# Kernel optimization log

Hardware: AMD Instinct MI355X
Metric: run time of the kernel (lower is better)

Reference implementation:

```python
import jax, jax.numpy as jnp
import numpy as np

N_NODES = 50000
N_EDGES = 800000
F_IN = 32
H = 128
LN_EPS = 1e-5


def _gcn_layer(h, src, tgt, w_self, b_self, w_neigh, b_neigh):
    # h: [N, D]; src/tgt: [E]
    n = h.shape[0]
    self_feat = h @ w_self + b_self                      # [N, Dout]
    src_feat = h[src]                                    # [E, D] gather
    agg = jax.ops.segment_sum(src_feat, tgt, num_segments=n)          # [N, D]
    cnt = jax.ops.segment_sum(jnp.ones((src.shape[0],), h.dtype), tgt,
                              num_segments=n)[:, None]   # [N, 1]
    agg = agg / jnp.maximum(cnt, 1.0)
    return self_feat + agg @ w_neigh + b_neigh


def _layer_norm(x, gamma, beta):
    mu = jnp.mean(x, axis=-1, keepdims=True)
    var = jnp.mean(jnp.square(x - mu), axis=-1, keepdims=True)
    return (x - mu) * jax.lax.rsqrt(var + LN_EPS) * gamma + beta


def setup_inputs() -> dict:
    key = jax.random.key(0)
    ks = jax.random.split(key, 16)
    s_in = 1.0 / np.sqrt(F_IN)
    s_h = 1.0 / np.sqrt(H)
    inp = {
        "x": jax.random.normal(ks[0], (N_NODES, F_IN), jnp.float32),
        "edge_index": jax.random.randint(ks[1], (2, N_EDGES), 0, N_NODES, jnp.int64)
        if jax.config.jax_enable_x64 else
        jax.random.randint(ks[1], (2, N_EDGES), 0, N_NODES, jnp.int32),
        "w_in": jax.random.uniform(ks[2], (F_IN, H), jnp.float32, -s_in, s_in),
        "b_in": jax.random.uniform(ks[3], (H,), jnp.float32, -s_in, s_in),
        "ws0": jax.random.uniform(ks[4], (H, H), jnp.float32, -s_h, s_h),
        "bs0": jax.random.uniform(ks[5], (H,), jnp.float32, -s_h, s_h),
        "wn0": jax.random.uniform(ks[6], (H, H), jnp.float32, -s_h, s_h),
        "bn0": jax.random.uniform(ks[7], (H,), jnp.float32, -s_h, s_h),
        "g0": jnp.ones((H,), jnp.float32),
        "be0": jnp.zeros((H,), jnp.float32),
        "ws1": jax.random.uniform(ks[8], (H, H), jnp.float32, -s_h, s_h),
        "bs1": jax.random.uniform(ks[9], (H,), jnp.float32, -s_h, s_h),
        "wn1": jax.random.uniform(ks[10], (H, H), jnp.float32, -s_h, s_h),
        "bn1": jax.random.uniform(ks[11], (H,), jnp.float32, -s_h, s_h),
        "g1": jnp.ones((H,), jnp.float32),
        "be1": jnp.zeros((H,), jnp.float32),
    }
    return inp


def reference(x, edge_index, w_in, b_in, ws0, bs0, wn0, bn0, g0, be0,
              ws1, bs1, wn1, bn1, g1, be1):
    src, tgt = edge_index[0], edge_index[1]
    h = jax.nn.relu(x @ w_in + b_in)                     # input_proj + relu
    # layer 0 (intermediate): gcn -> LN -> relu -> dropout(eval=id) -> residual
    residual = h
    h = _gcn_layer(h, src, tgt, ws0, bs0, wn0, bn0)
    h = _layer_norm(h, g0, be0)
    h = jax.nn.relu(h) + residual
    # layer 1 (final): gcn -> LN
    h = _gcn_layer(h, src, tgt, ws1, bs1, wn1, bn1)
    h = _layer_norm(h, g1, be1)
    return h
```

## Files before the change

kernel.cpp:

```cpp
#include <hip/hip_runtime.h>

#define H 128
#define CAP 64
typedef unsigned short ushort_t;
typedef __bf16 bf16x8 __attribute__((ext_vector_type(8)));
typedef unsigned short u16x8 __attribute__((ext_vector_type(8)));
typedef float f32x4 __attribute__((ext_vector_type(4)));
typedef float f32x2 __attribute__((ext_vector_type(2)));

__device__ __forceinline__ float bf2f(ushort_t b) {
    return __uint_as_float(((unsigned int)b) << 16);
}
__device__ __forceinline__ ushort_t f2bf(float f) {
    unsigned int u = __float_as_uint(f);
    unsigned int r = (u + 0x7fffu + ((u >> 16) & 1u)) >> 16;
    return (ushort_t)r;
}
__device__ __forceinline__ unsigned char f2fp8(float f) {
    int r = __builtin_amdgcn_cvt_pk_fp8_f32(f, f, 0, false);
    return (unsigned char)(r & 0xff);
}
__device__ __forceinline__ void acc8(float* s, uint2 v) {
    f32x2 a0 = __builtin_amdgcn_cvt_pk_f32_fp8(v.x, false);
    f32x2 a1 = __builtin_amdgcn_cvt_pk_f32_fp8(v.x, true);
    f32x2 a2 = __builtin_amdgcn_cvt_pk_f32_fp8(v.y, false);
    f32x2 a3 = __builtin_amdgcn_cvt_pk_f32_fp8(v.y, true);
    s[0] += a0.x; s[1] += a0.y; s[2] += a1.x; s[3] += a1.y;
    s[4] += a2.x; s[5] += a2.y; s[6] += a3.x; s[7] += a3.y;
}

__device__ __forceinline__
void pack_one(int idx, const float* __restrict__ W0, const float* __restrict__ W1,
              const float* __restrict__ b0, const float* __restrict__ b1,
              ushort_t* __restrict__ Wpack, float* __restrict__ bsum,
              int Ksplit, int K)
{
    int total = K * 16;
    if (idx < total) {
        int l = idx & 63, tt = (idx >> 6) & 7, s = idx >> 9;
        int c = tt * 16 + (l & 15);
        int kb = s * 32 + ((l >> 4) & 3) * 8;
#pragma unroll
        for (int j = 0; j < 8; ++j) {
            int k = kb + j;
            float v = (k < Ksplit) ? W0[(size_t)k * H + c]
                                   : W1[(size_t)(k - Ksplit) * H + c];
            Wpack[(size_t)idx * 8 + j] = f2bf(v);
        }
    }
    if (idx < H) bsum[idx] = b0[idx] + (b1 ? b1[idx] : 0.f);
}

__global__ __launch_bounds__(256)
void k_prep(const float* __restrict__ w_in, const float* __restrict__ b_in,
            const float* __restrict__ ws0, const float* __restrict__ bs0,
            const float* __restrict__ wn0, const float* __restrict__ bn0,
            const float* __restrict__ ws1, const float* __restrict__ bs1,
            const float* __restrict__ wn1, const float* __restrict__ bn1,
            ushort_t* __restrict__ Wpin, float* __restrict__ bin,
            ushort_t* __restrict__ Wp0, float* __restrict__ bsm0,
            ushort_t* __restrict__ Wp1, float* __restrict__ bsm1,
            int* __restrict__ fl, int N)
{
    int b = blockIdx.x, t = threadIdx.x;
    if (b < 2) {
        pack_one(b * 256 + t, w_in, w_in, b_in, nullptr, Wpin, bin, 32, 32);
    } else if (b < 18) {
        pack_one((b - 2) * 256 + t, ws0, wn0, bs0, bn0, Wp0, bsm0, 128, 256);
    } else if (b < 34) {
        pack_one((b - 18) * 256 + t, ws1, wn1, bs1, bn1, Wp1, bsm1, 128, 256);
    } else {
        int i = (b - 34) * 256 + t;
        if (i < N) fl[i] = 0;
    }
}

#define FILL_CHUNK 4096

__device__ __forceinline__
void fill_body(int blk, const int* __restrict__ srcs, const int* __restrict__ tgts,
               int* __restrict__ fl, ushort_t* __restrict__ col, int E)
{
    int range = blk & 7;
    int chunk = blk >> 3;
    int lim = chunk * FILL_CHUNK + FILL_CHUNK;
    if (lim > E) lim = E;
    for (int i = chunk * FILL_CHUNK + threadIdx.x; i < lim; i += 256) {
        int tt = tgts[i];
        if ((tt >> 13) == range) {
            int p = atomicAdd(&fl[tt], 1);
            if (p < CAP) col[tt * CAP + p] = (ushort_t)srcs[i];
        }
    }
}

template<int K, int DO_LN, int RESREL, int RELU, int OUTBF, int HQ, int AF32>
__device__ __forceinline__
void gemm_body(int bidm,
               const ushort_t* __restrict__ A, const float* __restrict__ Af, int lda,
               const ushort_t* __restrict__ Wpack,
               const float* __restrict__ bias,
               const float* __restrict__ g, const float* __restrict__ be,
               const ushort_t* __restrict__ resid, int ldr,
               float* __restrict__ Cf, ushort_t* __restrict__ Cb,
               unsigned char* __restrict__ hq, int ldc, int M)
{
    constexpr int NS = K / 32;
    __shared__ ushort_t Bs[NS * 8 * 64 * 8];
    const int t = threadIdx.x;
    {
        const uint4* wsrc = (const uint4*)Wpack;
        uint4* wdst = (uint4*)Bs;
        constexpr int CH = K * 16;
#pragma unroll
        for (int i = t; i < CH; i += 256) wdst[i] = wsrc[i];
    }
    __syncthreads();

    const int wave = t >> 6, lane = t & 63;
    const int quad = lane >> 4, l16 = lane & 15;
    const int m0 = bidm * 128 + wave * 32;

    f32x4 acc[2][8];
#pragma unroll
    for (int mt = 0; mt < 2; ++mt)
#pragma unroll
        for (int nt = 0; nt < 8; ++nt) acc[mt][nt] = (f32x4){0.f, 0.f, 0.f, 0.f};

    bf16x8 afrag[NS][2];
#pragma unroll
    for (int s = 0; s < NS; ++s)
#pragma unroll
        for (int mt = 0; mt < 2; ++mt) {
            int row = m0 + mt * 16 + l16;
            if (row >= M) row = M - 1;
            if (AF32) {
                const float* p = Af + (size_t)row * lda + s * 32 + quad * 8;
                float4 v0 = *(const float4*)p;
                float4 v1 = *(const float4*)(p + 4);
                union { u16x8 u; bf16x8 b; } cv;
                cv.u[0] = f2bf(v0.x); cv.u[1] = f2bf(v0.y);
                cv.u[2] = f2bf(v0.z); cv.u[3] = f2bf(v0.w);
                cv.u[4] = f2bf(v1.x); cv.u[5] = f2bf(v1.y);
                cv.u[6] = f2bf(v1.z); cv.u[7] = f2bf(v1.w);
                afrag[s][mt] = cv.b;
            } else {
                afrag[s][mt] = *(const bf16x8*)(A + (size_t)row * lda + s * 32 + quad * 8);
            }
        }

    const bf16x8* bfr = (const bf16x8*)Bs;
#pragma unroll
    for (int s = 0; s < NS; ++s)
#pragma unroll
        for (int nt = 0; nt < 8; ++nt) {
            bf16x8 b = bfr[(s * 8 + nt) * 64 + lane];
#pragma unroll
            for (int mt = 0; mt < 2; ++mt)
                acc[mt][nt] = __builtin_amdgcn_mfma_f32_16x16x32_bf16(
                    afrag[s][mt], b, acc[mt][nt], 0, 0, 0);
        }

    float bv[8], gv[8], bev[8];
#pragma unroll
    for (int nt = 0; nt < 8; ++nt) {
        int c = nt * 16 + l16;
        bv[nt] = bias[c];
        if (DO_LN) { gv[nt] = g[c]; bev[nt] = be[c]; }
    }

#pragma unroll
    for (int mt = 0; mt < 2; ++mt)
#pragma unroll
        for (int r = 0; r < 4; ++r) {
            int row = m0 + mt * 16 + quad * 4 + r;
            float v[8];
#pragma unroll
            for (int nt = 0; nt < 8; ++nt) v[nt] = acc[mt][nt][r] + bv[nt];
            if (DO_LN) {
                float s1 = 0.f, s2 = 0.f;
#pragma unroll
                for (int nt = 0; nt < 8; ++nt) { s1 += v[nt]; s2 += v[nt] * v[nt]; }
#pragma unroll
                for (int mk = 1; mk < 16; mk <<= 1) {
                    s1 += __shfl_xor(s1, mk);
                    s2 += __shfl_xor(s2, mk);
                }
                float mu = s1 * (1.f / H);
                float var = s2 * (1.f / H) - mu * mu;
                float rs = rsqrtf(var + 1e-5f);
#pragma unroll
                for (int nt = 0; nt < 8; ++nt)
                    v[nt] = (v[nt] - mu) * rs * gv[nt] + bev[nt];
            }
            if (row < M) {
#pragma unroll
                for (int nt = 0; nt < 8; ++nt) {
                    int c = nt * 16 + l16;
                    float y = v[nt];
                    if (RELU) y = fmaxf(y, 0.f);
                    if (RESREL)
                        y = fmaxf(y, 0.f) + bf2f(resid[(size_t)row * ldr + c]);
                    if (OUTBF) Cb[(size_t)row * ldc + c] = f2bf(y);
                    else       Cf[(size_t)row * ldc + c] = y;
                    if (HQ) hq[(size_t)row * H + c] = f2fp8(y);
                }
            }
        }
}

__global__ __launch_bounds__(256)
void k_gin(const float* __restrict__ x, const ushort_t* __restrict__ Wpin,
           const float* __restrict__ bin,
           ushort_t* __restrict__ Cb, unsigned char* __restrict__ hq,
           const int* __restrict__ srcs, const int* __restrict__ tgts,
           int* __restrict__ fl, ushort_t* __restrict__ col, int E,
           int fillBlocks, int M)
{
    if ((int)blockIdx.x < fillBlocks) {
        fill_body(blockIdx.x, srcs, tgts, fl, col, E);
        return;
    }
    gemm_body<32, 0, 0, 1, 1, 1, 1>(blockIdx.x - fillBlocks,
        nullptr, x, 32, Wpin, bin, nullptr, nullptr, nullptr, 0,
        nullptr, Cb, hq, 256, M);
}

__global__ __launch_bounds__(256)
void k_gl0(const ushort_t* __restrict__ A, const ushort_t* __restrict__ Wp,
           const float* __restrict__ bias,
           const float* __restrict__ g, const float* __restrict__ be,
           ushort_t* __restrict__ Cb, unsigned char* __restrict__ hq, int M)
{
    gemm_body<256, 1, 1, 0, 1, 1, 0>(blockIdx.x,
        A, nullptr, 256, Wp, bias, g, be, A, 256,
        nullptr, Cb, hq, 256, M);
}

__global__ __launch_bounds__(256)
void k_gl1(const ushort_t* __restrict__ A, const ushort_t* __restrict__ Wp,
           const float* __restrict__ bias,
           const float* __restrict__ g, const float* __restrict__ be,
           float* __restrict__ Cf, int M)
{
    gemm_body<256, 1, 0, 0, 0, 0, 0>(blockIdx.x,
        A, nullptr, 256, Wp, bias, g, be, nullptr, 0,
        Cf, nullptr, nullptr, H, M);
}

__device__ __forceinline__
void agg_body(int blk, const unsigned char* __restrict__ hq,
              const int* __restrict__ fl,
              const ushort_t* __restrict__ col, ushort_t* __restrict__ out, int n)
{
    int wave = threadIdx.x >> 6;
    int lane = threadIdx.x & 63;
    int grp = lane >> 4, li = lane & 15;
    int n0 = blk * 8 + wave * 2;
    if (n0 >= n) return;

    int cnt[2], m[2];
#pragma unroll
    for (int u = 0; u < 2; ++u) {
        int nd = n0 + u;
        cnt[u] = (nd < n) ? fl[nd] : 0;
        m[u] = cnt[u] < CAP ? cnt[u] : CAP;
    }
    float s[2][8];
#pragma unroll
    for (int u = 0; u < 2; ++u)
#pragma unroll
        for (int j = 0; j < 8; ++j) s[u][j] = 0.f;

    int mx = m[0] > m[1] ? m[0] : m[1];
    for (int e = 0; e < mx; e += 16) {
        uint2 v[2][4];
#pragma unroll
        for (int u = 0; u < 2; ++u)
#pragma unroll
            for (int q = 0; q < 4; ++q) {
                int idx = e + q * 4 + grp;
                bool val = idx < m[u];
                int r = val ? (int)col[(n0 + u) * CAP + idx] : 0;
                uint2 tv = {0u, 0u};
                if (val) tv = *(const uint2*)(hq + (size_t)r * 128 + li * 8);
                v[u][q] = tv;
            }
#pragma unroll
        for (int u = 0; u < 2; ++u)
#pragma unroll
            for (int q = 0; q < 4; ++q) acc8(s[u], v[u][q]);
    }
#pragma unroll
    for (int u = 0; u < 2; ++u)
#pragma unroll
        for (int j = 0; j < 8; ++j) {
            s[u][j] += __shfl_xor(s[u][j], 16);
            s[u][j] += __shfl_xor(s[u][j], 32);
        }
    if (grp < 2 && (n0 + grp) < n) {
        int u = grp;
        float inv = 1.f / fmaxf((float)cnt[u], 1.f);
        uint4 o;
        o.x = ((unsigned)f2bf(s[u][1] * inv) << 16) | f2bf(s[u][0] * inv);
        o.y = ((unsigned)f2bf(s[u][3] * inv) << 16) | f2bf(s[u][2] * inv);
        o.z = ((unsigned)f2bf(s[u][5] * inv) << 16) | f2bf(s[u][4] * inv);
        o.w = ((unsigned)f2bf(s[u][7] * inv) << 16) | f2bf(s[u][6] * inv);
        *(uint4*)(out + (size_t)(n0 + u) * 256 + li * 8) = o;
    }
}

__global__ __launch_bounds__(256)
void k_agg0(const unsigned char* __restrict__ hq, const int* __restrict__ fl,
            const ushort_t* __restrict__ col, ushort_t* __restrict__ out, int n)
{ agg_body(blockIdx.x, hq, fl, col, out, n); }

__global__ __launch_bounds__(256)
void k_agg1(const unsigned char* __restrict__ hq, const int* __restrict__ fl,
            const ushort_t* __restrict__ col, ushort_t* __restrict__ out, int n)
{ agg_body(blockIdx.x, hq, fl, col, out, n); }

extern "C" void kernel_launch(void* const* d_in, const int* in_sizes, int n_in,
                              void* d_out, int out_size, void* d_ws, size_t ws_size,
                              hipStream_t stream)
{
    const float* x    = (const float*)d_in[0];
    const int*   ei   = (const int*)d_in[1];
    const float* w_in = (const float*)d_in[2];
    const float* b_in = (const float*)d_in[3];
    const float* ws0  = (const float*)d_in[4];
    const float* bs0  = (const float*)d_in[5];
    const float* wn0  = (const float*)d_in[6];
    const float* bn0  = (const float*)d_in[7];
    const float* g0   = (const float*)d_in[8];
    const float* be0  = (const float*)d_in[9];
    const float* ws1  = (const float*)d_in[10];
    const float* bs1  = (const float*)d_in[11];
    const float* wn1  = (const float*)d_in[12];
    const float* bn1  = (const float*)d_in[13];
    const float* g1   = (const float*)d_in[14];
    const float* be1  = (const float*)d_in[15];

    const int N = in_sizes[0] / 32;
    const int E = in_sizes[1] / 2;
    const int* srcs = ei;
    const int* tgts = ei + E;

    char* w = (char*)d_ws;
    ushort_t* Acat0 = (ushort_t*)w;  w += (size_t)N * 256 * 2;
    ushort_t* Acat1 = (ushort_t*)w;  w += (size_t)N * 256 * 2;
    unsigned char* hq0 = (unsigned char*)w;  w += (size_t)N * H;
    unsigned char* hq1 = (unsigned char*)w;  w += (size_t)N * H;
    ushort_t* Wpin  = (ushort_t*)w;  w += 32 * H * 2;
    ushort_t* Wp0   = (ushort_t*)w;  w += 256 * H * 2;
    ushort_t* Wp1   = (ushort_t*)w;  w += 256 * H * 2;
    float* bin  = (float*)w;         w += H * 4;
    float* bsm0 = (float*)w;         w += H * 4;
    float* bsm1 = (float*)w;         w += H * 4;
    int* fl     = (int*)w;           w += (size_t)N * 4;
    ushort_t* col = (ushort_t*)w;    w += (size_t)N * CAP * 2;

    int gN = (N + 255) / 256;
    int gM = (N + 127) / 128;
    int gA = (N + 7) / 8;
    int gF = 8 * ((E + FILL_CHUNK - 1) / FILL_CHUNK);

    k_prep<<<34 + gN, 256, 0, stream>>>(
        w_in, b_in, ws0, bs0, wn0, bn0, ws1, bs1, wn1, bn1,
        Wpin, bin, Wp0, bsm0, Wp1, bsm1, fl, N);

    k_gin<<<gF + gM, 256, 0, stream>>>(
        x, Wpin, bin, Acat0, hq0, srcs, tgts, fl, col, E, gF, N);

    k_agg0<<<gA, 256, 0, stream>>>(hq0, fl, col, Acat0 + 128, N);
    k_gl0<<<gM, 256, 0, stream>>>(Acat0, Wp0, bsm0, g0, be0, Acat1, hq1, N);

    k_agg1<<<gA, 256, 0, stream>>>(hq1, fl, col, Acat1 + 128, N);
    k_gl1<<<gM, 256, 0, stream>>>(Acat1, Wp1, bsm1, g1, be1, (float*)d_out, N);
}
```

Before: 233.9 us.

## Fuse neighbor aggregation into the layer GEMM via shared-memory tile

Drops the separate aggregation kernels. Each layer kernel now gathers fp8 neighbor features for 64 rows, writes the bf16 means into a swizzled shared-memory tile, and feeds them straight to the MFMA GEMM together with the self features. This removes two launches and the global round trip of the aggregated half of the concatenated activation, and the activation buffers shrink to width H. In exchange each block does only a 64-row tile with 64KB of staged weights plus 16KB for the tile, which lowers occupancy, and the per-thread serial gather loop has less memory-level parallelism than the old wave-parallel edge split.

```diff
diff --git a/kernel.cpp b/kernel.cpp
--- a/kernel.cpp
+++ b/kernel.cpp
@@ -94,26 +94,18 @@
     }
 }
 
-template<int K, int DO_LN, int RESREL, int RELU, int OUTBF, int HQ, int AF32>
 __device__ __forceinline__
-void gemm_body(int bidm,
-               const ushort_t* __restrict__ A, const float* __restrict__ Af, int lda,
-               const ushort_t* __restrict__ Wpack,
-               const float* __restrict__ bias,
-               const float* __restrict__ g, const float* __restrict__ be,
-               const ushort_t* __restrict__ resid, int ldr,
-               float* __restrict__ Cf, ushort_t* __restrict__ Cb,
-               unsigned char* __restrict__ hq, int ldc, int M)
-{
-    constexpr int NS = K / 32;
-    __shared__ ushort_t Bs[NS * 8 * 64 * 8];
+void gin_gemm(int bidm, const float* __restrict__ Af,
+              const ushort_t* __restrict__ Wpack, const float* __restrict__ bias,
+              ushort_t* __restrict__ Cb, unsigned char* __restrict__ hq, int M)
+{
+    __shared__ ushort_t Bs[8 * 64 * 8];
     const int t = threadIdx.x;
     {
         const uint4* wsrc = (const uint4*)Wpack;
         uint4* wdst = (uint4*)Bs;
-        constexpr int CH = K * 16;
-#pragma unroll
-        for (int i = t; i < CH; i += 256) wdst[i] = wsrc[i];
+#pragma unroll
+        for (int i = t; i < 512; i += 256) wdst[i] = wsrc[i];
     }
     __syncthreads();
 
@@ -127,83 +119,48 @@
 #pragma unroll
         for (int nt = 0; nt < 8; ++nt) acc[mt][nt] = (f32x4){0.f, 0.f, 0.f, 0.f};
 
-    bf16x8 afrag[NS][2];
-#pragma unroll
-    for (int s = 0; s < NS; ++s)
-#pragma unroll
-        for (int mt = 0; mt < 2; ++mt) {
-            int row = m0 + mt * 16 + l16;
-            if (row >= M) row = M - 1;
-            if (AF32) {
-                const float* p = Af + (size_t)row * lda + s * 32 + quad * 8;
-                float4 v0 = *(const float4*)p;
-                float4 v1 = *(const float4*)(p + 4);
-                union { u16x8 u; bf16x8 b; } cv;
-                cv.u[0] = f2bf(v0.x); cv.u[1] = f2bf(v0.y);
-                cv.u[2] = f2bf(v0.z); cv.u[3] = f2bf(v0.w);
-                cv.u[4] = f2bf(v1.x); cv.u[5] = f2bf(v1.y);
-                cv.u[6] = f2bf(v1.z); cv.u[7] = f2bf(v1.w);
-                afrag[s][mt] = cv.b;
-            } else {
-                afrag[s][mt] = *(const bf16x8*)(A + (size_t)row * lda + s * 32 + quad * 8);
-            }
-        }
+    bf16x8 afrag[2];
+#pragma unroll
+    for (int mt = 0; mt < 2; ++mt) {
+        int row = m0 + mt * 16 + l16;
+        if (row >= M) row = M - 1;
+        const float* p = Af + (size_t)row * 32 + quad * 8;
+        float4 v0 = *(const float4*)p;
+        float4 v1 = *(const float4*)(p + 4);
+        union { u16x8 u; bf16x8 b; } cv;
+        cv.u[0] = f2bf(v0.x); cv.u[1] = f2bf(v0.y);
+        cv.u[2] = f2bf(v0.z); cv.u[3] = f2bf(v0.w);
+        cv.u[4] = f2bf(v1.x); cv.u[5] = f2bf(v1.y);
+        cv.u[6] = f2bf(v1.z); cv.u[7] = f2bf(v1.w);
+        afrag[mt] = cv.b;
+    }
 
     const bf16x8* bfr = (const bf16x8*)Bs;
 #pragma unroll
-    for (int s = 0; s < NS; ++s)
-#pragma unroll
-        for (int nt = 0; nt < 8; ++nt) {
-            bf16x8 b = bfr[(s * 8 + nt) * 64 + lane];
-#pragma unroll
-            for (int mt = 0; mt < 2; ++mt)
-                acc[mt][nt] = __builtin_amdgcn_mfma_f32_16x16x32_bf16(
-                    afrag[s][mt], b, acc[mt][nt], 0, 0, 0);
-        }
-
-    float bv[8], gv[8], bev[8];
-#pragma unroll
     for (int nt = 0; nt < 8; ++nt) {
-        int c = nt * 16 + l16;
-        bv[nt] = bias[c];
-        if (DO_LN) { gv[nt] = g[c]; bev[nt] = be[c]; }
-    }
+        bf16x8 b = bfr[nt * 64 + lane];
+#pragma unroll
+        for (int mt = 0; mt < 2; ++mt)
+            acc[mt][nt] = __builtin_amdgcn_mfma_f32_16x16x32_bf16(
+                afrag[mt], b, acc[mt][nt], 0, 0, 0);
+    }
+
+    float bv[8];
+#pragma unroll
+    for (int nt = 0; nt < 8; ++nt) bv[nt] = bias[nt * 16 + l16];
 
 #pragma unroll
     for (int mt = 0; mt < 2; ++mt)
 #pragma unroll
         for (int r = 0; r < 4; ++r) {
             int row = m0 + mt * 16 + quad * 4 + r;
-            float v[8];
-#pragma unroll
-            for (int nt = 0; nt < 8; ++nt) v[nt] = acc[mt][nt][r] + bv[nt];
-            if (DO_LN) {
-                float s1 = 0.f, s2 = 0.f;
-#pragma unroll
-                for (int nt = 0; nt < 8; ++nt) { s1 += v[nt]; s2 += v[nt] * v[nt]; }
-#pragma unroll
-                for (int mk = 1; mk < 16; mk <<= 1) {
-                    s1 += __shfl_xor(s1, mk);
-                    s2 += __shfl_xor(s2, mk);
-                }
-                float mu = s1 * (1.f / H);
-                float var = s2 * (1.f / H) - mu * mu;
-                float rs = rsqrtf(var + 1e-5f);
-#pragma unroll
-                for (int nt = 0; nt < 8; ++nt)
-                    v[nt] = (v[nt] - mu) * rs * gv[nt] + bev[nt];
-            }
             if (row < M) {
 #pragma unroll
                 for (int nt = 0; nt < 8; ++nt) {
                     int c = nt * 16 + l16;
-                    float y = v[nt];
-                    if (RELU) y = fmaxf(y, 0.f);
-                    if (RESREL)
-                        y = fmaxf(y, 0.f) + bf2f(resid[(size_t)row * ldr + c]);
-                    if (OUTBF) Cb[(size_t)row * ldc + c] = f2bf(y);
-                    else       Cf[(size_t)row * ldc + c] = y;
-                    if (HQ) hq[(size_t)row * H + c] = f2fp8(y);
+                    float y = fmaxf(acc[mt][nt][r] + bv[nt], 0.f);
+                    Cb[(size_t)row * H + c] = f2bf(y);
+                    hq[(size_t)row * H + c] = f2fp8(y);
                 }
             }
         }
@@ -221,104 +178,168 @@
         fill_body(blockIdx.x, srcs, tgts, fl, col, E);
         return;
     }
-    gemm_body<32, 0, 0, 1, 1, 1, 1>(blockIdx.x - fillBlocks,
-        nullptr, x, 32, Wpin, bin, nullptr, nullptr, nullptr, 0,
-        nullptr, Cb, hq, 256, M);
+    gin_gemm(blockIdx.x - fillBlocks, x, Wpin, bin, Cb, hq, M);
+}
+
+template<int RESREL, int OUTBF, int HQ>
+__device__ __forceinline__
+void gla_body(int bidm, const ushort_t* __restrict__ A,
+              const unsigned char* __restrict__ hq_in,
+              const int* __restrict__ fl, const ushort_t* __restrict__ col,
+              const ushort_t* __restrict__ Wpack,
+              const float* __restrict__ bias,
+              const float* __restrict__ g, const float* __restrict__ be,
+              const ushort_t* __restrict__ resid,
+              float* __restrict__ Cf, ushort_t* __restrict__ Cb,
+              unsigned char* __restrict__ hq_out, int M)
+{
+    __shared__ ushort_t Bs[8 * 8 * 64 * 8];
+    __shared__ ushort_t Ag[64 * 128];
+    const int t = threadIdx.x;
+
+    {
+        const uint4* wsrc = (const uint4*)Wpack;
+        uint4* wdst = (uint4*)Bs;
+#pragma unroll
+        for (int i = t; i < 4096; i += 256) wdst[i] = wsrc[i];
+    }
+
+    {
+        const int gid = t >> 4, li = t & 15;
+        const int base = bidm * 64;
+#pragma unroll
+        for (int k = 0; k < 4; ++k) {
+            int lr = gid * 4 + k;
+            int nd = base + lr;
+            int cnt = (nd < M) ? fl[nd] : 0;
+            int m = cnt < CAP ? cnt : CAP;
+            float s[8];
+#pragma unroll
+            for (int j = 0; j < 8; ++j) s[j] = 0.f;
+            const ushort_t* cl = col + (size_t)nd * CAP;
+            int e = 0;
+            for (; e + 4 <= m; e += 4) {
+                int r0 = cl[e], r1 = cl[e + 1], r2 = cl[e + 2], r3 = cl[e + 3];
+                uint2 v0 = *(const uint2*)(hq_in + (size_t)r0 * 128 + li * 8);
+                uint2 v1 = *(const uint2*)(hq_in + (size_t)r1 * 128 + li * 8);
+                uint2 v2 = *(const uint2*)(hq_in + (size_t)r2 * 128 + li * 8);
+                uint2 v3 = *(const uint2*)(hq_in + (size_t)r3 * 128 + li * 8);
+                acc8(s, v0); acc8(s, v1); acc8(s, v2); acc8(s, v3);
+            }
+            for (; e < m; ++e) {
+                int r = cl[e];
+                uint2 v = *(const uint2*)(hq_in + (size_t)r * 128 + li * 8);
+                acc8(s, v);
+            }
+            float inv = 1.f / fmaxf((float)cnt, 1.f);
+            uint4 o;
+            o.x = ((unsigned)f2bf(s[1] * inv) << 16) | f2bf(s[0] * inv);
+            o.y = ((unsigned)f2bf(s[3] * inv) << 16) | f2bf(s[2] * inv);
+            o.z = ((unsigned)f2bf(s[5] * inv) << 16) | f2bf(s[4] * inv);
+            o.w = ((unsigned)f2bf(s[7] * inv) << 16) | f2bf(s[6] * inv);
+            int boff = (lr * 256 + li * 16) ^ ((lr & 7) << 4);
+            *(uint4*)((char*)Ag + boff) = o;
+        }
+    }
+    __syncthreads();
+
+    const int wave = t >> 6, lane = t & 63;
+    const int quad = lane >> 4, l16 = lane & 15;
+    const int m0 = bidm * 64 + wave * 16;
+
+    f32x4 acc[8];
+#pragma unroll
+    for (int nt = 0; nt < 8; ++nt) acc[nt] = (f32x4){0.f, 0.f, 0.f, 0.f};
+
+    bf16x8 afrag[8];
+    {
+        int row = m0 + l16;
+        if (row >= M) row = M - 1;
+#pragma unroll
+        for (int s = 0; s < 4; ++s)
+            afrag[s] = *(const bf16x8*)(A + (size_t)row * H + s * 32 + quad * 8);
+        int lw = wave * 16 + l16;
+#pragma unroll
+        for (int s = 4; s < 8; ++s) {
+            int boff = (lw * 256 + (s - 4) * 64 + quad * 16) ^ ((lw & 7) << 4);
+            afrag[s] = *(const bf16x8*)((const char*)Ag + boff);
+        }
+    }
+
+    const bf16x8* bfr = (const bf16x8*)Bs;
+#pragma unroll
+    for (int s = 0; s < 8; ++s)
+#pragma unroll
+        for (int nt = 0; nt < 8; ++nt) {
+            bf16x8 b = bfr[(s * 8 + nt) * 64 + lane];
+            acc[nt] = __builtin_amdgcn_mfma_f32_16x16x32_bf16(
+                afrag[s], b, acc[nt], 0, 0, 0);
+        }
+
+    float bv[8], gv[8], bev[8];
+#pragma unroll
+    for (int nt = 0; nt < 8; ++nt) {
+        int c = nt * 16 + l16;
+        bv[nt] = bias[c];
+        gv[nt] = g[c]; bev[nt] = be[c];
+    }
+
+#pragma unroll
+    for (int r = 0; r < 4; ++r) {
+        int row = m0 + quad * 4 + r;
+        float v[8];
+#pragma unroll
+        for (int nt = 0; nt < 8; ++nt) v[nt] = acc[nt][r] + bv[nt];
+        float s1 = 0.f, s2 = 0.f;
+#pragma unroll
+        for (int nt = 0; nt < 8; ++nt) { s1 += v[nt]; s2 += v[nt] * v[nt]; }
+#pragma unroll
+        for (int mk = 1; mk < 16; mk <<= 1) {
+            s1 += __shfl_xor(s1, mk);
+            s2 += __shfl_xor(s2, mk);
+        }
+        float mu = s1 * (1.f / H);
+        float var = s2 * (1.f / H) - mu * mu;
+        float rs = rsqrtf(var + 1e-5f);
+#pragma unroll
+        for (int nt = 0; nt < 8; ++nt)
+            v[nt] = (v[nt] - mu) * rs * gv[nt] + bev[nt];
+        if (row < M) {
+#pragma unroll
+            for (int nt = 0; nt < 8; ++nt) {
+                int c = nt * 16 + l16;
+                float y = v[nt];
+                if (RESREL) y = fmaxf(y, 0.f) + bf2f(resid[(size_t)row * H + c]);
+                if (OUTBF) Cb[(size_t)row * H + c] = f2bf(y);
+                else       Cf[(size_t)row * H + c] = y;
+                if (HQ) hq_out[(size_t)row * H + c] = f2fp8(y);
+            }
+        }
+    }
 }
 
 __global__ __launch_bounds__(256)
-void k_gl0(const ushort_t* __restrict__ A, const ushort_t* __restrict__ Wp,
-           const float* __restrict__ bias,
-           const float* __restrict__ g, const float* __restrict__ be,
-           ushort_t* __restrict__ Cb, unsigned char* __restrict__ hq, int M)
-{
-    gemm_body<256, 1, 1, 0, 1, 1, 0>(blockIdx.x,
-        A, nullptr, 256, Wp, bias, g, be, A, 256,
-        nullptr, Cb, hq, 256, M);
+void k_gla0(const ushort_t* __restrict__ A, const unsigned char* __restrict__ hq_in,
+            const int* __restrict__ fl, const ushort_t* __restrict__ col,
+            const ushort_t* __restrict__ Wp, const float* __restrict__ bias,
+            const float* __restrict__ g, const float* __restrict__ be,
+            const ushort_t* __restrict__ resid,
+            ushort_t* __restrict__ Cb, unsigned char* __restrict__ hq_out, int M)
+{
+    gla_body<1, 1, 1>(blockIdx.x, A, hq_in, fl, col, Wp, bias, g, be, resid,
+                      nullptr, Cb, hq_out, M);
 }
 
 __global__ __launch_bounds__(256)
-void k_gl1(const ushort_t* __restrict__ A, const ushort_t* __restrict__ Wp,
-           const float* __restrict__ bias,
-           const float* __restrict__ g, const float* __restrict__ be,
-           float* __restrict__ Cf, int M)
-{
-    gemm_body<256, 1, 0, 0, 0, 0, 0>(blockIdx.x,
-        A, nullptr, 256, Wp, bias, g, be, nullptr, 0,
-        Cf, nullptr, nullptr, H, M);
-}
-
-__device__ __forceinline__
-void agg_body(int blk, const unsigned char* __restrict__ hq,
-              const int* __restrict__ fl,
-              const ushort_t* __restrict__ col, ushort_t* __restrict__ out, int n)
-{
-    int wave = threadIdx.x >> 6;
-    int lane = threadIdx.x & 63;
-    int grp = lane >> 4, li = lane & 15;
-    int n0 = blk * 8 + wave * 2;
-    if (n0 >= n) return;
-
-    int cnt[2], m[2];
-#pragma unroll
-    for (int u = 0; u < 2; ++u) {
-        int nd = n0 + u;
-        cnt[u] = (nd < n) ? fl[nd] : 0;
-        m[u] = cnt[u] < CAP ? cnt[u] : CAP;
-    }
-    float s[2][8];
-#pragma unroll
-    for (int u = 0; u < 2; ++u)
-#pragma unroll
-        for (int j = 0; j < 8; ++j) s[u][j] = 0.f;
-
-    int mx = m[0] > m[1] ? m[0] : m[1];
-    for (int e = 0; e < mx; e += 16) {
-        uint2 v[2][4];
-#pragma unroll
-        for (int u = 0; u < 2; ++u)
-#pragma unroll
-            for (int q = 0; q < 4; ++q) {
-                int idx = e + q * 4 + grp;
-                bool val = idx < m[u];
-                int r = val ? (int)col[(n0 + u) * CAP + idx] : 0;
-                uint2 tv = {0u, 0u};
-                if (val) tv = *(const uint2*)(hq + (size_t)r * 128 + li * 8);
-                v[u][q] = tv;
-            }
-#pragma unroll
-        for (int u = 0; u < 2; ++u)
-#pragma unroll
-            for (int q = 0; q < 4; ++q) acc8(s[u], v[u][q]);
-    }
-#pragma unroll
-    for (int u = 0; u < 2; ++u)
-#pragma unroll
-        for (int j = 0; j < 8; ++j) {
-            s[u][j] += __shfl_xor(s[u][j], 16);
-            s[u][j] += __shfl_xor(s[u][j], 32);
-        }
-    if (grp < 2 && (n0 + grp) < n) {
-        int u = grp;
-        float inv = 1.f / fmaxf((float)cnt[u], 1.f);
-        uint4 o;
-        o.x = ((unsigned)f2bf(s[u][1] * inv) << 16) | f2bf(s[u][0] * inv);
-        o.y = ((unsigned)f2bf(s[u][3] * inv) << 16) | f2bf(s[u][2] * inv);
-        o.z = ((unsigned)f2bf(s[u][5] * inv) << 16) | f2bf(s[u][4] * inv);
-        o.w = ((unsigned)f2bf(s[u][7] * inv) << 16) | f2bf(s[u][6] * inv);
-        *(uint4*)(out + (size_t)(n0 + u) * 256 + li * 8) = o;
-    }
-}
-
-__global__ __launch_bounds__(256)
-void k_agg0(const unsigned char* __restrict__ hq, const int* __restrict__ fl,
-            const ushort_t* __restrict__ col, ushort_t* __restrict__ out, int n)
-{ agg_body(blockIdx.x, hq, fl, col, out, n); }
-
-__global__ __launch_bounds__(256)
-void k_agg1(const unsigned char* __restrict__ hq, const int* __restrict__ fl,
-            const ushort_t* __restrict__ col, ushort_t* __restrict__ out, int n)
-{ agg_body(blockIdx.x, hq, fl, col, out, n); }
+void k_gla1(const ushort_t* __restrict__ A, const unsigned char* __restrict__ hq_in,
+            const int* __restrict__ fl, const ushort_t* __restrict__ col,
+            const ushort_t* __restrict__ Wp, const float* __restrict__ bias,
+            const float* __restrict__ g, const float* __restrict__ be,
+            float* __restrict__ Cf, int M)
+{
+    gla_body<0, 0, 0>(blockIdx.x, A, hq_in, fl, col, Wp, bias, g, be, nullptr,
+                      Cf, nullptr, nullptr, M);
+}
 
 extern "C" void kernel_launch(void* const* d_in, const int* in_sizes, int n_in,
                               void* d_out, int out_size, void* d_ws, size_t ws_size,
@@ -347,8 +368,8 @@
     const int* tgts = ei + E;
 
     char* w = (char*)d_ws;
-    ushort_t* Acat0 = (ushort_t*)w;  w += (size_t)N * 256 * 2;
-    ushort_t* Acat1 = (ushort_t*)w;  w += (size_t)N * 256 * 2;
+    ushort_t* h0 = (ushort_t*)w;     w += (size_t)N * H * 2;
+    ushort_t* h1 = (ushort_t*)w;     w += (size_t)N * H * 2;
     unsigned char* hq0 = (unsigned char*)w;  w += (size_t)N * H;
     unsigned char* hq1 = (unsigned char*)w;  w += (size_t)N * H;
     ushort_t* Wpin  = (ushort_t*)w;  w += 32 * H * 2;
@@ -362,7 +383,7 @@
 
     int gN = (N + 255) / 256;
     int gM = (N + 127) / 128;
-    int gA = (N + 7) / 8;
+    int gG = (N + 63) / 64;
     int gF = 8 * ((E + FILL_CHUNK - 1) / FILL_CHUNK);
 
     k_prep<<<34 + gN, 256, 0, stream>>>(
@@ -370,11 +391,11 @@
         Wpin, bin, Wp0, bsm0, Wp1, bsm1, fl, N);
 
     k_gin<<<gF + gM, 256, 0, stream>>>(
-        x, Wpin, bin, Acat0, hq0, srcs, tgts, fl, col, E, gF, N);
-
-    k_agg0<<<gA, 256, 0, stream>>>(hq0, fl, col, Acat0 + 128, N);
-    k_gl0<<<gM, 256, 0, stream>>>(Acat0, Wp0, bsm0, g0, be0, Acat1, hq1, N);
-
-    k_agg1<<<gA, 256, 0, stream>>>(hq1, fl, col, Acat1 + 128, N);
-    k_gl1<<<gM, 256, 0, stream>>>(Acat1, Wp1, bsm1, g1, be1, (float*)d_out, N);
-}
+        x, Wpin, bin, h0, hq0, srcs, tgts, fl, col, E, gF, N);
+
+    k_gla0<<<gG, 256, 0, stream>>>(
+        h0, hq0, fl, col, Wp0, bsm0, g0, be0, h0, h1, hq1, N);
+
+    k_gla1<<<gG, 256, 0, stream>>>(
+        h1, hq1, fl, col, Wp1, bsm1, g1, be1, (float*)d_out, N);
+}
```

New measurement: 261.1 us. 1.12x slower.
